# Performance work log

Hardware: AMD Instinct MI355X
Metric: run time of the kernel (lower is better)

## Reference

```python
import jax, jax.numpy as jnp
import numpy as np

N, D, H, O = 512, 128, 256, 256

def setup_inputs() -> dict:
    key = jax.random.key(0)
    ks = jax.random.split(key, 10)
    s = lambda fan_in: 1.0 / np.sqrt(fan_in)
    return {
        "x": jax.random.normal(ks[0], (N, D), dtype=jnp.float32),
        "adj": jax.random.uniform(ks[1], (N, N), dtype=jnp.float32),
        # mpnn_compute: MLP(2D -> H -> H)
        "W1": jax.random.normal(ks[2], (H, 2 * D), dtype=jnp.float32) * s(2 * D),
        "b1": jnp.zeros((H,), dtype=jnp.float32),
        "W2": jax.random.normal(ks[3], (H, H), dtype=jnp.float32) * s(H),
        "b2": jnp.zeros((H,), dtype=jnp.float32),
        # out_compute: MLP(H -> H -> O)
        "Wo1": jax.random.normal(ks[4], (H, H), dtype=jnp.float32) * s(H),
        "bo1": jnp.zeros((H,), dtype=jnp.float32),
        "Wo2": jax.random.normal(ks[5], (O, H), dtype=jnp.float32) * s(H),
        "bo2": jnp.zeros((O,), dtype=jnp.float32),
    }


def reference(x, adj, W1, b1, W2, b2, Wo1, bo1, Wo2, bo2):
    n, d = x.shape
    # e[i, j] = concat(x[j], x[i]); split W1 so we never materialize the cat:
    # linear_1(e)[i,j] = x[j] @ Wa^T + x[i] @ Wb^T + b1
    Wa = W1[:, :d]   # acts on x[j] (first half of cat = x1 = x broadcast over i)
    Wb = W1[:, d:]   # acts on x[i] (second half = x2)
    pa = x @ Wa.T    # [N, H], indexed by j
    pb = x @ Wb.T    # [N, H], indexed by i
    h = jax.nn.relu(pa[None, :, :] + pb[:, None, :] + b1)  # [N, N, H]
    e = jnp.einsum('ijh,kh->ijk', h, W2) + b2               # [N, N, H]
    pred = jnp.mean(adj[:, :, None] * e, axis=1)            # [N, H]
    # out_compute MLP (normalize_input=False)
    h2 = jax.nn.relu(pred @ Wo1.T + bo1)
    return h2 @ Wo2.T + bo2                                  # [N, O]
```

## Files before the change

kernel.cpp:

```cpp
#include <hip/hip_runtime.h>

#define NN 512
#define DD 128
#define HH 256

__global__ __launch_bounds__(256) void k0_tr(const float* __restrict__ W1,
                                             const float* __restrict__ W2,
                                             const float* __restrict__ Wo1,
                                             const float* __restrict__ Wo2,
                                             float* __restrict__ wsT) {
    __shared__ float tl[64][68];
    const int b = blockIdx.x;
    const int t = threadIdx.x;
    const int m = b >> 4, tile = b & 15;
    const float* src = (m == 0) ? W1 : (m == 1) ? W2 : (m == 2) ? Wo1 : Wo2;
    float* dst = wsT + m * (HH * HH);
    const int sr0 = (tile >> 2) * 64;
    const int sc0 = (tile & 3) * 64;
    const int rr = t >> 4;
    const int cc = (t & 15) * 4;
    #pragma unroll
    for (int it = 0; it < 4; ++it) {
        const int row = rr + 16 * it;
        float4 v = *(const float4*)&src[(sr0 + row) * HH + sc0 + cc];
        tl[row][cc + 0] = v.x;
        tl[row][cc + 1] = v.y;
        tl[row][cc + 2] = v.z;
        tl[row][cc + 3] = v.w;
    }
    __syncthreads();
    #pragma unroll
    for (int it = 0; it < 4; ++it) {
        const int lc = rr + 16 * it;
        float4 o;
        o.x = tl[cc + 0][lc];
        o.y = tl[cc + 1][lc];
        o.z = tl[cc + 2][lc];
        o.w = tl[cc + 3][lc];
        *(float4*)&dst[(sc0 + lc) * HH + sr0 + cc] = o;
    }
}

__global__ __launch_bounds__(256) void k1_papb(const float* __restrict__ x,
                                               const float* __restrict__ W1T,
                                               const float* __restrict__ b1,
                                               float* __restrict__ pa,
                                               float* __restrict__ pbb) {
    __shared__ float xs[2][DD];
    const int b = blockIdx.x;
    const int t = threadIdx.x;
    const int i0 = b * 2;
    if (t < 64) {
        const int f = t * 4;
        *(float4*)&xs[f >> 7][f & 127] = *(const float4*)&x[i0 * DD + f];
    }
    __syncthreads();
    const float* wt = W1T + t;
    const int crot = (b * 8) & 127;
    float pe0 = 0.f, po0 = 0.f, pe1 = 0.f, po1 = 0.f;
    float qe0 = 0.f, qo0 = 0.f, qe1 = 0.f, qo1 = 0.f;
    #pragma unroll 2
    for (int cc0 = 0; cc0 < 128; cc0 += 8) {
        const int c = (cc0 + crot) & 127;
        float w0 = wt[(c + 0) * HH], w1 = wt[(c + 1) * HH];
        float w2 = wt[(c + 2) * HH], w3 = wt[(c + 3) * HH];
        float w4 = wt[(c + 4) * HH], w5 = wt[(c + 5) * HH];
        float w6 = wt[(c + 6) * HH], w7 = wt[(c + 7) * HH];
        float v0 = wt[(128 + c + 0) * HH], v1 = wt[(128 + c + 1) * HH];
        float v2 = wt[(128 + c + 2) * HH], v3 = wt[(128 + c + 3) * HH];
        float v4 = wt[(128 + c + 4) * HH], v5 = wt[(128 + c + 5) * HH];
        float v6 = wt[(128 + c + 6) * HH], v7 = wt[(128 + c + 7) * HH];
        float4 x0a = *(const float4*)&xs[0][c];
        float4 x0b = *(const float4*)&xs[0][c + 4];
        float4 x1a = *(const float4*)&xs[1][c];
        float4 x1b = *(const float4*)&xs[1][c + 4];
        pe0 += w0 * x0a.x + w1 * x0a.y + w2 * x0a.z + w3 * x0a.w;
        po0 += w4 * x0b.x + w5 * x0b.y + w6 * x0b.z + w7 * x0b.w;
        pe1 += w0 * x1a.x + w1 * x1a.y + w2 * x1a.z + w3 * x1a.w;
        po1 += w4 * x1b.x + w5 * x1b.y + w6 * x1b.z + w7 * x1b.w;
        qe0 += v0 * x0a.x + v1 * x0a.y + v2 * x0a.z + v3 * x0a.w;
        qo0 += v4 * x0b.x + v5 * x0b.y + v6 * x0b.z + v7 * x0b.w;
        qe1 += v0 * x1a.x + v1 * x1a.y + v2 * x1a.z + v3 * x1a.w;
        qo1 += v4 * x1b.x + v5 * x1b.y + v6 * x1b.z + v7 * x1b.w;
    }
    const float bb = b1[t];
    pa[i0 * HH + t] = pe0 + po0;
    pa[(i0 + 1) * HH + t] = pe1 + po1;
    pbb[i0 * HH + t] = qe0 + qo0 + bb;
    pbb[(i0 + 1) * HH + t] = qe1 + qo1 + bb;
}

__device__ __forceinline__ void stage_dot8(const float* __restrict__ wt,
                                           const float* in0, const float* in1,
                                           int hrot, float& A0, float& A1) {
    float e0 = 0.f, o0 = 0.f, e1 = 0.f, o1 = 0.f;
    #pragma unroll 2
    for (int hh0 = 0; hh0 < 64; hh0 += 8) {
        const int hh = (hh0 + hrot) & 63;
        float w0 = wt[(hh + 0) * HH], w1 = wt[(hh + 1) * HH];
        float w2 = wt[(hh + 2) * HH], w3 = wt[(hh + 3) * HH];
        float w4 = wt[(hh + 4) * HH], w5 = wt[(hh + 5) * HH];
        float w6 = wt[(hh + 6) * HH], w7 = wt[(hh + 7) * HH];
        float4 t0a = *(const float4*)&in0[hh];
        float4 t0b = *(const float4*)&in0[hh + 4];
        float4 t1a = *(const float4*)&in1[hh];
        float4 t1b = *(const float4*)&in1[hh + 4];
        e0 += w0 * t0a.x + w1 * t0a.y + w2 * t0a.z + w3 * t0a.w;
        o0 += w4 * t0b.x + w5 * t0b.y + w6 * t0b.z + w7 * t0b.w;
        e1 += w0 * t1a.x + w1 * t1a.y + w2 * t1a.z + w3 * t1a.w;
        o1 += w4 * t1b.x + w5 * t1b.y + w6 * t1b.z + w7 * t1b.w;
    }
    A0 = e0 + o0;
    A1 = e1 + o1;
}

__global__ __launch_bounds__(1024) void k2_rest(const float* __restrict__ adj,
                                                const float* __restrict__ pa,
                                                const float* __restrict__ pbb,
                                                const float* __restrict__ wsT,
                                                const float* __restrict__ b2,
                                                const float* __restrict__ bo1,
                                                const float* __restrict__ bo2,
                                                float* __restrict__ out) {
    __shared__ float adjs[2][NN];
    __shared__ float pbbs[2][HH];
    __shared__ float ts[2][HH];
    __shared__ float buf1[2][HH];
    __shared__ float buf2[2][HH];
    __shared__ float redbuf[2048];
    __shared__ float rsum_s[2];

    const int b = blockIdx.x;
    const int t = threadIdx.x;
    const int i0 = b * 2;

    if (t < 256) {
        const int f = t * 4;
        *(float4*)&adjs[f >> 9][f & 511] = *(const float4*)&adj[(i0 + (f >> 9)) * NN + (f & 511)];
    } else if (t < 384) {
        const int f = (t - 256) * 4;
        *(float4*)&pbbs[f >> 8][f & 255] = *(const float4*)&pbb[(i0 + (f >> 8)) * HH + (f & 255)];
    }
    __syncthreads();

    if (t < 128) {
        const int r = t >> 6, l = t & 63;
        float s = 0.f;
        #pragma unroll
        for (int m = 0; m < 8; ++m) s += adjs[r][l + 64 * m];
        #pragma unroll
        for (int off = 32; off > 0; off >>= 1) s += __shfl_down(s, off, 64);
        if (l == 0) rsum_s[r] = s;
    }

    {
        const int hb = t >> 9;
        const int jq = (t >> 7) & 3;
        const int hl = t & 127;
        const int h = hb * 128 + hl;
        const float pb0 = pbbs[0][h];
        const float pb1 = pbbs[1][h];
        const float* pac = pa + (jq * 128) * HH + h;
        const float* arow0 = &adjs[0][jq * 128];
        const float* arow1 = &adjs[1][jq * 128];
        const int jrot = (b * 8) & 127;
        float ae0 = 0.f, ao0 = 0.f, ae1 = 0.f, ao1 = 0.f;
        #pragma unroll 2
        for (int jj0 = 0; jj0 < 128; jj0 += 8) {
            const int j = (jj0 + jrot) & 127;
            float p0 = pac[(j + 0) * HH], p1 = pac[(j + 1) * HH];
            float p2 = pac[(j + 2) * HH], p3 = pac[(j + 3) * HH];
            float p4 = pac[(j + 4) * HH], p5 = pac[(j + 5) * HH];
            float p6 = pac[(j + 6) * HH], p7 = pac[(j + 7) * HH];
            float4 A0a = *(const float4*)&arow0[j];
            float4 A0b = *(const float4*)&arow0[j + 4];
            float4 A1a = *(const float4*)&arow1[j];
            float4 A1b = *(const float4*)&arow1[j + 4];
            float r0 = fmaxf(p0 + pb0, 0.f), r1 = fmaxf(p1 + pb0, 0.f);
            float r2 = fmaxf(p2 + pb0, 0.f), r3 = fmaxf(p3 + pb0, 0.f);
            float r4 = fmaxf(p4 + pb0, 0.f), r5 = fmaxf(p5 + pb0, 0.f);
            float r6 = fmaxf(p6 + pb0, 0.f), r7 = fmaxf(p7 + pb0, 0.f);
            ae0 += A0a.x * r0 + A0a.y * r1 + A0a.z * r2 + A0a.w * r3;
            ao0 += A0b.x * r4 + A0b.y * r5 + A0b.z * r6 + A0b.w * r7;
            float s0 = fmaxf(p0 + pb1, 0.f), s1 = fmaxf(p1 + pb1, 0.f);
            float s2 = fmaxf(p2 + pb1, 0.f), s3 = fmaxf(p3 + pb1, 0.f);
            float s4 = fmaxf(p4 + pb1, 0.f), s5 = fmaxf(p5 + pb1, 0.f);
            float s6 = fmaxf(p6 + pb1, 0.f), s7 = fmaxf(p7 + pb1, 0.f);
            ae1 += A1a.x * s0 + A1a.y * s1 + A1a.z * s2 + A1a.w * s3;
            ao1 += A1b.x * s4 + A1b.y * s5 + A1b.z * s6 + A1b.w * s7;
        }
        redbuf[((jq * 2 + hb) * 2 + 0) * 128 + hl] = ae0 + ao0;
        redbuf[((jq * 2 + hb) * 2 + 1) * 128 + hl] = ae1 + ao1;
        __syncthreads();
        if (jq < 2) {
            const int r = jq;
            float s = 0.f;
            #pragma unroll
            for (int q = 0; q < 4; ++q)
                s += redbuf[((q * 2 + hb) * 2 + r) * 128 + hl];
            ts[r][h] = s;
        }
    }
    __syncthreads();

    const int k = t & 255;
    const int hp = t >> 8;
    const int hrot = (b * 8) & 63;
    const float* W2T  = wsT + 1 * (HH * HH);
    const float* Wo1T = wsT + 2 * (HH * HH);
    const float* Wo2T = wsT + 3 * (HH * HH);

    {
        float a0, a1;
        stage_dot8(W2T + (hp * 64) * HH + k, &ts[0][hp * 64], &ts[1][hp * 64], hrot, a0, a1);
        redbuf[(hp * 2 + 0) * 256 + k] = a0;
        redbuf[(hp * 2 + 1) * 256 + k] = a1;
        __syncthreads();
        if (hp < 2) {
            const int r = hp;
            float s = 0.f;
            #pragma unroll
            for (int p = 0; p < 4; ++p) s += redbuf[(p * 2 + r) * 256 + k];
            buf1[r][k] = (s + b2[k] * rsum_s[r]) * (1.0f / (float)NN);
        }
    }
    __syncthreads();

    {
        float a0, a1;
        stage_dot8(Wo1T + (hp * 64) * HH + k, &buf1[0][hp * 64], &buf1[1][hp * 64], hrot, a0, a1);
        redbuf[(hp * 2 + 0) * 256 + k] = a0;
        redbuf[(hp * 2 + 1) * 256 + k] = a1;
        __syncthreads();
        if (hp < 2) {
            const int r = hp;
            float s = 0.f;
            #pragma unroll
            for (int p = 0; p < 4; ++p) s += redbuf[(p * 2 + r) * 256 + k];
            buf2[r][k] = fmaxf(s + bo1[k], 0.f);
        }
    }
    __syncthreads();

    {
        float a0, a1;
        stage_dot8(Wo2T + (hp * 64) * HH + k, &buf2[0][hp * 64], &buf2[1][hp * 64], hrot, a0, a1);
        redbuf[(hp * 2 + 0) * 256 + k] = a0;
        redbuf[(hp * 2 + 1) * 256 + k] = a1;
        __syncthreads();
        if (hp < 2) {
            const int r = hp;
            float s = 0.f;
            #pragma unroll
            for (int p = 0; p < 4; ++p) s += redbuf[(p * 2 + r) * 256 + k];
            out[(i0 + r) * HH + k] = s + bo2[k];
        }
    }
}

extern "C" void kernel_launch(void* const* d_in, const int* in_sizes, int n_in,
                              void* d_out, int out_size, void* d_ws, size_t ws_size,
                              hipStream_t stream) {
    const float* x   = (const float*)d_in[0];
    const float* adj = (const float*)d_in[1];
    const float* W1  = (const float*)d_in[2];
    const float* b1  = (const float*)d_in[3];
    const float* W2  = (const float*)d_in[4];
    const float* b2  = (const float*)d_in[5];
    const float* Wo1 = (const float*)d_in[6];
    const float* bo1 = (const float*)d_in[7];
    const float* Wo2 = (const float*)d_in[8];
    const float* bo2 = (const float*)d_in[9];
    float* out = (float*)d_out;
    float* ws  = (float*)d_ws;

    float* wsT = ws;
    float* pa  = ws + 262144;
    float* pbb = ws + 393216;

    k0_tr<<<64, 256, 0, stream>>>(W1, W2, Wo1, Wo2, wsT);
    k1_papb<<<256, 256, 0, stream>>>(x, wsT, b1, pa, pbb);
    k2_rest<<<256, 1024, 0, stream>>>(adj, pa, pbb, wsT, b2, bo1, bo2, out);
}
```

Before: 32.81 us.

## Vectorize k2_rest loads to float4 per thread with wider split-K reduction

Each thread in k2_rest now handles four consecutive output columns, reading pa and the transposed weights as float4 in place of scalar strided loads. In exchange, the reduction dimension is split across 16 slices instead of 4. The aim is fewer, wider global memory transactions and fewer address computations per useful FMA. The cost is a larger shared reduction buffer (32 KB), a 16-way final sum, and removal of the per-block rotation of the weight stages.

```diff
diff --git a/kernel.cpp b/kernel.cpp
--- a/kernel.cpp
+++ b/kernel.cpp
@@ -90,30 +90,6 @@
     pbb[(i0 + 1) * HH + t] = qe1 + qo1 + bb;
 }
 
-__device__ __forceinline__ void stage_dot8(const float* __restrict__ wt,
-                                           const float* in0, const float* in1,
-                                           int hrot, float& A0, float& A1) {
-    float e0 = 0.f, o0 = 0.f, e1 = 0.f, o1 = 0.f;
-    #pragma unroll 2
-    for (int hh0 = 0; hh0 < 64; hh0 += 8) {
-        const int hh = (hh0 + hrot) & 63;
-        float w0 = wt[(hh + 0) * HH], w1 = wt[(hh + 1) * HH];
-        float w2 = wt[(hh + 2) * HH], w3 = wt[(hh + 3) * HH];
-        float w4 = wt[(hh + 4) * HH], w5 = wt[(hh + 5) * HH];
-        float w6 = wt[(hh + 6) * HH], w7 = wt[(hh + 7) * HH];
-        float4 t0a = *(const float4*)&in0[hh];
-        float4 t0b = *(const float4*)&in0[hh + 4];
-        float4 t1a = *(const float4*)&in1[hh];
-        float4 t1b = *(const float4*)&in1[hh + 4];
-        e0 += w0 * t0a.x + w1 * t0a.y + w2 * t0a.z + w3 * t0a.w;
-        o0 += w4 * t0b.x + w5 * t0b.y + w6 * t0b.z + w7 * t0b.w;
-        e1 += w0 * t1a.x + w1 * t1a.y + w2 * t1a.z + w3 * t1a.w;
-        o1 += w4 * t1b.x + w5 * t1b.y + w6 * t1b.z + w7 * t1b.w;
-    }
-    A0 = e0 + o0;
-    A1 = e1 + o1;
-}
-
 __global__ __launch_bounds__(1024) void k2_rest(const float* __restrict__ adj,
                                                 const float* __restrict__ pa,
                                                 const float* __restrict__ pbb,
@@ -123,11 +99,11 @@
                                                 const float* __restrict__ bo2,
                                                 float* __restrict__ out) {
     __shared__ float adjs[2][NN];
-    __shared__ float pbbs[2][HH];
+    __shared__ float4 pbbs4[2][64];
     __shared__ float ts[2][HH];
     __shared__ float buf1[2][HH];
     __shared__ float buf2[2][HH];
-    __shared__ float redbuf[2048];
+    __shared__ float redbuf[8192];
     __shared__ float rsum_s[2];
 
     const int b = blockIdx.x;
@@ -138,8 +114,9 @@
         const int f = t * 4;
         *(float4*)&adjs[f >> 9][f & 511] = *(const float4*)&adj[(i0 + (f >> 9)) * NN + (f & 511)];
     } else if (t < 384) {
-        const int f = (t - 256) * 4;
-        *(float4*)&pbbs[f >> 8][f & 255] = *(const float4*)&pbb[(i0 + (f >> 8)) * HH + (f & 255)];
+        const int u = t - 256;
+        const int r = u >> 6, q = u & 63;
+        pbbs4[r][q] = *(const float4*)&pbb[(i0 + r) * HH + q * 4];
     }
     __syncthreads();
 
@@ -154,105 +131,117 @@
     }
 
     {
-        const int hb = t >> 9;
-        const int jq = (t >> 7) & 3;
-        const int hl = t & 127;
-        const int h = hb * 128 + hl;
-        const float pb0 = pbbs[0][h];
-        const float pb1 = pbbs[1][h];
-        const float* pac = pa + (jq * 128) * HH + h;
-        const float* arow0 = &adjs[0][jq * 128];
-        const float* arow1 = &adjs[1][jq * 128];
-        const int jrot = (b * 8) & 127;
-        float ae0 = 0.f, ao0 = 0.f, ae1 = 0.f, ao1 = 0.f;
-        #pragma unroll 2
-        for (int jj0 = 0; jj0 < 128; jj0 += 8) {
-            const int j = (jj0 + jrot) & 127;
-            float p0 = pac[(j + 0) * HH], p1 = pac[(j + 1) * HH];
-            float p2 = pac[(j + 2) * HH], p3 = pac[(j + 3) * HH];
-            float p4 = pac[(j + 4) * HH], p5 = pac[(j + 5) * HH];
-            float p6 = pac[(j + 6) * HH], p7 = pac[(j + 7) * HH];
-            float4 A0a = *(const float4*)&arow0[j];
-            float4 A0b = *(const float4*)&arow0[j + 4];
-            float4 A1a = *(const float4*)&arow1[j];
-            float4 A1b = *(const float4*)&arow1[j + 4];
-            float r0 = fmaxf(p0 + pb0, 0.f), r1 = fmaxf(p1 + pb0, 0.f);
-            float r2 = fmaxf(p2 + pb0, 0.f), r3 = fmaxf(p3 + pb0, 0.f);
-            float r4 = fmaxf(p4 + pb0, 0.f), r5 = fmaxf(p5 + pb0, 0.f);
-            float r6 = fmaxf(p6 + pb0, 0.f), r7 = fmaxf(p7 + pb0, 0.f);
-            ae0 += A0a.x * r0 + A0a.y * r1 + A0a.z * r2 + A0a.w * r3;
-            ao0 += A0b.x * r4 + A0b.y * r5 + A0b.z * r6 + A0b.w * r7;
-            float s0 = fmaxf(p0 + pb1, 0.f), s1 = fmaxf(p1 + pb1, 0.f);
-            float s2 = fmaxf(p2 + pb1, 0.f), s3 = fmaxf(p3 + pb1, 0.f);
-            float s4 = fmaxf(p4 + pb1, 0.f), s5 = fmaxf(p5 + pb1, 0.f);
-            float s6 = fmaxf(p6 + pb1, 0.f), s7 = fmaxf(p7 + pb1, 0.f);
-            ae1 += A1a.x * s0 + A1a.y * s1 + A1a.z * s2 + A1a.w * s3;
-            ao1 += A1b.x * s4 + A1b.y * s5 + A1b.z * s6 + A1b.w * s7;
-        }
-        redbuf[((jq * 2 + hb) * 2 + 0) * 128 + hl] = ae0 + ao0;
-        redbuf[((jq * 2 + hb) * 2 + 1) * 128 + hl] = ae1 + ao1;
-        __syncthreads();
-        if (jq < 2) {
-            const int r = jq;
-            float s = 0.f;
-            #pragma unroll
-            for (int q = 0; q < 4; ++q)
-                s += redbuf[((q * 2 + hb) * 2 + r) * 128 + hl];
+        const int hq = t & 63;
+        const int js = t >> 6;
+        const float4 pb0 = pbbs4[0][hq];
+        const float4 pb1 = pbbs4[1][hq];
+        float4 ac0 = {0.f, 0.f, 0.f, 0.f};
+        float4 ac1 = {0.f, 0.f, 0.f, 0.f};
+        #pragma unroll 4
+        for (int jj = 0; jj < 32; ++jj) {
+            const int j = js * 32 + ((jj + b) & 31);
+            float4 p = *(const float4*)&pa[j * HH + hq * 4];
+            const float a0 = adjs[0][j];
+            const float a1 = adjs[1][j];
+            float4 q0, q1;
+            q0.x = fmaxf(p.x + pb0.x, 0.f); q0.y = fmaxf(p.y + pb0.y, 0.f);
+            q0.z = fmaxf(p.z + pb0.z, 0.f); q0.w = fmaxf(p.w + pb0.w, 0.f);
+            q1.x = fmaxf(p.x + pb1.x, 0.f); q1.y = fmaxf(p.y + pb1.y, 0.f);
+            q1.z = fmaxf(p.z + pb1.z, 0.f); q1.w = fmaxf(p.w + pb1.w, 0.f);
+            ac0.x += a0 * q0.x; ac0.y += a0 * q0.y;
+            ac0.z += a0 * q0.z; ac0.w += a0 * q0.w;
+            ac1.x += a1 * q1.x; ac1.y += a1 * q1.y;
+            ac1.z += a1 * q1.z; ac1.w += a1 * q1.w;
+        }
+        *(float4*)&redbuf[(js * 2 + 0) * 256 + hq * 4] = ac0;
+        *(float4*)&redbuf[(js * 2 + 1) * 256 + hq * 4] = ac1;
+        __syncthreads();
+        if (t < 512) {
+            const int r = t >> 8, h = t & 255;
+            float s = 0.f;
+            #pragma unroll
+            for (int q = 0; q < 16; ++q) s += redbuf[(q * 2 + r) * 256 + h];
             ts[r][h] = s;
         }
     }
     __syncthreads();
 
-    const int k = t & 255;
-    const int hp = t >> 8;
-    const int hrot = (b * 8) & 63;
+    const int kq = t & 63;
+    const int hp = t >> 6;
     const float* W2T  = wsT + 1 * (HH * HH);
     const float* Wo1T = wsT + 2 * (HH * HH);
     const float* Wo2T = wsT + 3 * (HH * HH);
 
     {
-        float a0, a1;
-        stage_dot8(W2T + (hp * 64) * HH + k, &ts[0][hp * 64], &ts[1][hp * 64], hrot, a0, a1);
-        redbuf[(hp * 2 + 0) * 256 + k] = a0;
-        redbuf[(hp * 2 + 1) * 256 + k] = a1;
-        __syncthreads();
-        if (hp < 2) {
-            const int r = hp;
-            float s = 0.f;
-            #pragma unroll
-            for (int p = 0; p < 4; ++p) s += redbuf[(p * 2 + r) * 256 + k];
+        float4 a0 = {0.f, 0.f, 0.f, 0.f};
+        float4 a1 = {0.f, 0.f, 0.f, 0.f};
+        #pragma unroll 4
+        for (int hh = 0; hh < 16; ++hh) {
+            const int h = hp * 16 + hh;
+            float4 w = *(const float4*)&W2T[h * HH + kq * 4];
+            const float v0 = ts[0][h];
+            const float v1 = ts[1][h];
+            a0.x += w.x * v0; a0.y += w.y * v0; a0.z += w.z * v0; a0.w += w.w * v0;
+            a1.x += w.x * v1; a1.y += w.y * v1; a1.z += w.z * v1; a1.w += w.w * v1;
+        }
+        *(float4*)&redbuf[(hp * 2 + 0) * 256 + kq * 4] = a0;
+        *(float4*)&redbuf[(hp * 2 + 1) * 256 + kq * 4] = a1;
+        __syncthreads();
+        if (t < 512) {
+            const int r = t >> 8, k = t & 255;
+            float s = 0.f;
+            #pragma unroll
+            for (int p = 0; p < 16; ++p) s += redbuf[(p * 2 + r) * 256 + k];
             buf1[r][k] = (s + b2[k] * rsum_s[r]) * (1.0f / (float)NN);
         }
     }
     __syncthreads();
 
     {
-        float a0, a1;
-        stage_dot8(Wo1T + (hp * 64) * HH + k, &buf1[0][hp * 64], &buf1[1][hp * 64], hrot, a0, a1);
-        redbuf[(hp * 2 + 0) * 256 + k] = a0;
-        redbuf[(hp * 2 + 1) * 256 + k] = a1;
-        __syncthreads();
-        if (hp < 2) {
-            const int r = hp;
-            float s = 0.f;
-            #pragma unroll
-            for (int p = 0; p < 4; ++p) s += redbuf[(p * 2 + r) * 256 + k];
+        float4 a0 = {0.f, 0.f, 0.f, 0.f};
+        float4 a1 = {0.f, 0.f, 0.f, 0.f};
+        #pragma unroll 4
+        for (int hh = 0; hh < 16; ++hh) {
+            const int h = hp * 16 + hh;
+            float4 w = *(const float4*)&Wo1T[h * HH + kq * 4];
+            const float v0 = buf1[0][h];
+            const float v1 = buf1[1][h];
+            a0.x += w.x * v0; a0.y += w.y * v0; a0.z += w.z * v0; a0.w += w.w * v0;
+            a1.x += w.x * v1; a1.y += w.y * v1; a1.z += w.z * v1; a1.w += w.w * v1;
+        }
+        *(float4*)&redbuf[(hp * 2 + 0) * 256 + kq * 4] = a0;
+        *(float4*)&redbuf[(hp * 2 + 1) * 256 + kq * 4] = a1;
+        __syncthreads();
+        if (t < 512) {
+            const int r = t >> 8, k = t & 255;
+            float s = 0.f;
+            #pragma unroll
+            for (int p = 0; p < 16; ++p) s += redbuf[(p * 2 + r) * 256 + k];
             buf2[r][k] = fmaxf(s + bo1[k], 0.f);
         }
     }
     __syncthreads();
 
     {
-        float a0, a1;
-        stage_dot8(Wo2T + (hp * 64) * HH + k, &buf2[0][hp * 64], &buf2[1][hp * 64], hrot, a0, a1);
-        redbuf[(hp * 2 + 0) * 256 + k] = a0;
-        redbuf[(hp * 2 + 1) * 256 + k] = a1;
-        __syncthreads();
-        if (hp < 2) {
-            const int r = hp;
-            float s = 0.f;
-            #pragma unroll
-            for (int p = 0; p < 4; ++p) s += redbuf[(p * 2 + r) * 256 + k];
+        float4 a0 = {0.f, 0.f, 0.f, 0.f};
+        float4 a1 = {0.f, 0.f, 0.f, 0.f};
+        #pragma unroll 4
+        for (int hh = 0; hh < 16; ++hh) {
+            const int h = hp * 16 + hh;
+            float4 w = *(const float4*)&Wo2T[h * HH + kq * 4];
+            const float v0 = buf2[0][h];
+            const float v1 = buf2[1][h];
+            a0.x += w.x * v0; a0.y += w.y * v0; a0.z += w.z * v0; a0.w += w.w * v0;
+            a1.x += w.x * v1; a1.y += w.y * v1; a1.z += w.z * v1; a1.w += w.w * v1;
+        }
+        *(float4*)&redbuf[(hp * 2 + 0) * 256 + kq * 4] = a0;
+        *(float4*)&redbuf[(hp * 2 + 1) * 256 + kq * 4] = a1;
+        __syncthreads();
+        if (t < 512) {
+            const int r = t >> 8, k = t & 255;
+            float s = 0.f;
+            #pragma unroll
+            for (int p = 0; p < 16; ++p) s += redbuf[(p * 2 + r) * 256 + k];
             out[(i0 + r) * HH + k] = s + bo2[k];
         }
     }
```

Measured after the change: 30.94 us. 1.06x faster.
